# Kernel tuning notes

Hardware: AMD Instinct MI355X
Metric: run time of the kernel (lower is better)

Reference implementation:

```python
import jax, jax.numpy as jnp
import numpy as np


def setup_inputs() -> dict:
    key = jax.random.key(0)
    k1, k2, k3, k4 = jax.random.split(key, 4)
    B, T, N, D = 4, 8, 512, 256
    BT = B * T
    x = jax.random.normal(k1, (BT, N, D), dtype=jnp.float32)
    A_causal = jax.random.uniform(k2, (B, N, N), dtype=jnp.float32)
    W_qkv = jax.random.normal(k3, (3 * D, D), dtype=jnp.float32) * (D ** -0.5)
    W_proj = jax.random.normal(k4, (D, D), dtype=jnp.float32) * (D ** -0.5)
    b_proj = jnp.zeros((D,), dtype=jnp.float32)
    causal_lambda = jnp.ones((1,), dtype=jnp.float32) * 0.1
    return {
        "x": x,
        "A_causal": A_causal,
        "W_qkv": W_qkv,
        "W_proj": W_proj,
        "b_proj": b_proj,
        "causal_lambda": causal_lambda,
        "num_frames": 8,
    }


def reference(x, A_causal, W_qkv, W_proj, b_proj, causal_lambda, num_frames):
    BT, N, D = x.shape
    H = 8
    hd = D // H
    scale = hd ** -0.5
    # qkv projection (torch Linear: x @ W.T), split into q,k,v of shape [BT,H,N,hd]
    qkv = (x @ W_qkv.T).reshape(BT, N, 3, H, hd)
    qkv = jnp.transpose(qkv, (2, 0, 3, 1, 4))  # [3,BT,H,N,hd]
    q, k, v = qkv[0], qkv[1], qkv[2]
    attn = jnp.einsum("bhnd,bhmd->bhnm", q, k) * scale  # [BT,H,N,N]
    # expand A_causal [B,N,N] over frames (axis 0) and heads (broadcast axis 1)
    A_exp = jnp.repeat(A_causal, num_frames, axis=0)[:, None, :, :]  # [BT,1,N,N]
    attn = attn + causal_lambda[0] * A_exp
    attn = jax.nn.softmax(attn, axis=-1)
    out = jnp.einsum("bhnm,bhmd->bhnd", attn, v)  # [BT,H,N,hd]
    out = jnp.transpose(out, (0, 2, 1, 3)).reshape(BT, N, D)
    return out @ W_proj.T + b_proj
```

## Files before the change

kernel.cpp:

```cpp
#include <hip/hip_runtime.h>
#include <hip/hip_bf16.h>

typedef unsigned short u16;
typedef unsigned int   u32;
typedef __attribute__((ext_vector_type(8))) short short8;
typedef __attribute__((ext_vector_type(4))) float f32x4;

#define LOG2E 1.4426950408889634f
#define LDK 72

static __device__ __forceinline__ u16 f2b(float f) {
    u32 u = __float_as_uint(f);
    u += 0x7fffu + ((u >> 16) & 1u);
    return (u16)(u >> 16);
}
static __device__ __forceinline__ u32 pk2(float a, float b) {
    return (u32)f2b(a) | ((u32)f2b(b) << 16);
}
static __device__ __forceinline__ u32 cvtpk2(float a, float b) {
    u32 r;
    asm("v_cvt_pk_bf16_f32 %0, %1, %2" : "=v"(r) : "v"(b), "v"(a));
    return r;
}

__global__ __launch_bounds__(256) void prep(const float* __restrict__ X,
                                            const float* __restrict__ A,
                                            const float* __restrict__ LAM,
                                            const float* __restrict__ Wq,
                                            const float* __restrict__ Wp,
                                            u16* __restrict__ xb,
                                            u16* __restrict__ AB,
                                            u16* __restrict__ wqb,
                                            u16* __restrict__ wpb) {
    const int bid = blockIdx.x;
    const float* src;
    u16* dst;
    float scale;
    int base;
    if (bid < 2048)      { src = X;  dst = xb;  scale = 1.0f;            base = bid * 2048; }
    else if (bid < 2560) { src = A;  dst = AB;  scale = LAM[0] * LOG2E;  base = (bid - 2048) * 2048; }
    else if (bid < 2656) { src = Wq; dst = wqb; scale = 1.0f;            base = (bid - 2560) * 2048; }
    else                 { src = Wp; dst = wpb; scale = 1.0f;            base = (bid - 2656) * 2048; }
    const int i = base + threadIdx.x * 8;
    const float4 a = *(const float4*)(src + i);
    const float4 b = *(const float4*)(src + i + 4);
    uint4 o;
    o.x = pk2(scale * a.x, scale * a.y);
    o.y = pk2(scale * a.z, scale * a.w);
    o.z = pk2(scale * b.x, scale * b.y);
    o.w = pk2(scale * b.z, scale * b.w);
    *(uint4*)(dst + i) = o;
}

__global__ __launch_bounds__(256) void qkv_gemm(const u16* __restrict__ XB,
                                                const u16* __restrict__ WB,
                                                u16* __restrict__ qo,
                                                u16* __restrict__ ko,
                                                u16* __restrict__ vt) {
    __shared__ u16 SH[2 * 128 * LDK];
    u16* Xs = SH;
    u16* Ws = SH + 128 * LDK;
    const int t    = threadIdx.x;
    const int m0   = blockIdx.x << 7;
    const int o0   = blockIdx.y << 7;
    const int lane = t & 63;
    const int wid  = t >> 6;
    const int wr   = (wid >> 1) << 6;
    const int wc   = (wid & 1) << 6;
    const int ln   = lane & 15;
    const int quad = lane >> 4;

    const int r  = t >> 1;
    const int hf = (t & 1) << 5;
    const u16* xg = XB + (size_t)(m0 + r) * 256 + hf;
    const u16* wg = WB + (size_t)(o0 + r) * 256 + hf;
    uint4* xls = (uint4*)&Xs[r * LDK + hf];
    uint4* wls = (uint4*)&Ws[r * LDK + hf];

    f32x4 acc[4][4] = {};

    for (int kc = 0; kc < 256; kc += 64) {
        const uint4* xp = (const uint4*)(xg + kc);
        const uint4* wp = (const uint4*)(wg + kc);
        uint4 x0 = xp[0], x1 = xp[1], x2 = xp[2], x3 = xp[3];
        uint4 w0 = wp[0], w1 = wp[1], w2 = wp[2], w3 = wp[3];
        __syncthreads();
        xls[0] = x0; xls[1] = x1; xls[2] = x2; xls[3] = x3;
        wls[0] = w0; wls[1] = w1; wls[2] = w2; wls[3] = w3;
        __syncthreads();
#pragma unroll
        for (int kk = 0; kk < 64; kk += 32) {
            short8 a[4], b[4];
#pragma unroll
            for (int i = 0; i < 4; ++i)
                a[i] = *(const short8*)&Xs[(wr + i * 16 + ln) * LDK + kk + quad * 8];
#pragma unroll
            for (int j = 0; j < 4; ++j)
                b[j] = *(const short8*)&Ws[(wc + j * 16 + ln) * LDK + kk + quad * 8];
#pragma unroll
            for (int i = 0; i < 4; ++i)
#pragma unroll
                for (int j = 0; j < 4; ++j)
                    acc[i][j] = __builtin_amdgcn_mfma_f32_16x16x32_bf16(a[i], b[j], acc[i][j], 0, 0, 0);
        }
    }

    const int which = o0 >> 8;
    if (which < 2) {
        const float qscale = (which == 0) ? 0.17677669529663689f * LOG2E : 1.0f;
        u16* dst = (which == 0) ? qo : ko;
#pragma unroll
        for (int i = 0; i < 4; ++i) {
            const int mb = m0 + wr + i * 16 + quad * 4;
#pragma unroll
            for (int j = 0; j < 4; ++j) {
                const int o   = o0 + wc + j * 16 + ln;
                const int rem = o & 255;
                const int hh  = rem >> 5;
                const int dd  = rem & 31;
#pragma unroll
                for (int rr = 0; rr < 4; ++rr) {
                    const int m  = mb + rr;
                    const int bt = m >> 9;
                    const int n  = m & 511;
                    dst[(((size_t)bt * 8 + hh) * 512 + n) * 32 + dd] = f2b(acc[i][j][rr] * qscale);
                }
            }
        }
    } else {
        __syncthreads();
        u16* T = SH;
#pragma unroll
        for (int i = 0; i < 4; ++i) {
            const int ml = wr + i * 16 + quad * 4;
#pragma unroll
            for (int j = 0; j < 4; ++j) {
                const int ol = wc + j * 16 + ln;
                uint2 pv;
                pv.x = cvtpk2(acc[i][j][0], acc[i][j][1]);
                pv.y = cvtpk2(acc[i][j][2], acc[i][j][3]);
                *(uint2*)&T[ol * 136 + ml] = pv;
            }
        }
        __syncthreads();
        const int row = t >> 1;
        const int seg = (t & 1) << 6;
        const int o   = o0 + row;
        const int rem = o & 255;
        const int hh  = rem >> 5;
        const int dd  = rem & 31;
        const int bt  = m0 >> 9;
        u16* dstv = vt + (((size_t)bt * 8 + hh) * 32 + dd) * 512 + (m0 & 511) + seg;
#pragma unroll
        for (int kk2 = 0; kk2 < 8; ++kk2) {
            uint4 val = *(const uint4*)&T[row * 136 + seg + kk2 * 8];
            *(uint4*)(dstv + kk2 * 8) = val;
        }
    }
}

__global__ __launch_bounds__(256, 4) void attn_mfma(const u16* __restrict__ Q,
                                                    const u16* __restrict__ K,
                                                    const u16* __restrict__ VT,
                                                    const u16* __restrict__ AB,
                                                    const int* __restrict__ NF,
                                                    u16* __restrict__ AO) {
    __shared__ u16 Ks[2][64 * 40];
    __shared__ u16 Vs[2][32 * 72];
    __shared__ u16 Ps[4][32 * 40];
    const int t    = threadIdx.x;
    const int w    = t >> 6;
    const int lane = t & 63;
    const int ln   = lane & 15;
    const int quad = lane >> 4;
    const int L    = blockIdx.x;
    const int rr_  = L >> 3;
    const int qt   = rr_ & 3;
    const int h    = (rr_ >> 2) & 7;
    const int bt   = (L & 7) * 4 + (rr_ >> 5);
    const int bh   = bt * 8 + h;
    const int q0   = qt * 128 + w * 32;
    const size_t base = (size_t)bh * (512 * 32);
    const int b    = bt / NF[0];
    const u16* Ab  = AB + (size_t)b * 512 * 512;
    const u16* Ar0 = Ab + (size_t)(q0 + ln) * 512 + quad * 4;
    const u16* Ar1 = Ab + (size_t)(q0 + 16 + ln) * 512 + quad * 4;

    const int krow = t >> 2, kcol = (t & 3) * 8;
    const int vd   = t >> 3, vn   = (t & 7) * 8;
    const u16* Kg = K + base;
    const u16* Vg = VT + base;

    {
        uint4 s0 = *(const uint4*)(Kg + (size_t)krow * 32 + kcol);
        uint4 s2 = *(const uint4*)(Vg + (size_t)vd * 512 + vn);
        *(uint4*)&Ks[0][krow * 40 + kcol] = s0;
        *(uint4*)&Vs[0][vd * 72 + vn]     = s2;
    }
    uint2 ar[8];
#pragma unroll
    for (int mt = 0; mt < 4; ++mt) {
        ar[2*mt]     = *(const uint2*)(Ar0 + mt * 16);
        ar[2*mt + 1] = *(const uint2*)(Ar1 + mt * 16);
    }

    short8 qf[2];
#pragma unroll
    for (int nt = 0; nt < 2; ++nt)
        qf[nt] = *(const short8*)(Q + base + (size_t)(q0 + nt * 16 + ln) * 32 + quad * 8);

    f32x4 o[2][2] = {};
    float lsum0 = 0.f, lsum1 = 0.f;
    __syncthreads();

    int cur = 0;
    for (int jt = 0; jt < 512; jt += 64) {
        const int nxt = cur ^ 1;
        const int jn  = (jt + 64) & 511;
        uint4 t0 = *(const uint4*)(Kg + (size_t)(jn + krow) * 32 + kcol);
        uint4 t2 = *(const uint4*)(Vg + (size_t)vd * 512 + jn + vn);
        uint2 arn[8];
#pragma unroll
        for (int mt = 0; mt < 4; ++mt) {
            arn[2*mt]     = *(const uint2*)(Ar0 + jn + mt * 16);
            arn[2*mt + 1] = *(const uint2*)(Ar1 + jn + mt * 16);
        }

#pragma unroll
        for (int ks = 0; ks < 2; ++ks) {
#pragma unroll
            for (int mm = 0; mm < 2; ++mm) {
                const int mt = 2 * ks + mm;
                short8 ka = *(const short8*)&Ks[cur][(mt * 16 + ln) * 40 + quad * 8];
                f32x4 c0, c1;
                c0[0] = __uint_as_float(ar[2*mt].x << 16);   c0[1] = __uint_as_float(ar[2*mt].x & 0xffff0000u);
                c0[2] = __uint_as_float(ar[2*mt].y << 16);   c0[3] = __uint_as_float(ar[2*mt].y & 0xffff0000u);
                c1[0] = __uint_as_float(ar[2*mt+1].x << 16); c1[1] = __uint_as_float(ar[2*mt+1].x & 0xffff0000u);
                c1[2] = __uint_as_float(ar[2*mt+1].y << 16); c1[3] = __uint_as_float(ar[2*mt+1].y & 0xffff0000u);
                __builtin_amdgcn_s_setprio(1);
                const f32x4 s0 = __builtin_amdgcn_mfma_f32_16x16x32_bf16(ka, qf[0], c0, 0, 0, 0);
                const f32x4 s1 = __builtin_amdgcn_mfma_f32_16x16x32_bf16(ka, qf[1], c1, 0, 0, 0);
                __builtin_amdgcn_s_setprio(0);
                const float p00 = __builtin_amdgcn_exp2f(s0[0]), p01 = __builtin_amdgcn_exp2f(s0[1]);
                const float p02 = __builtin_amdgcn_exp2f(s0[2]), p03 = __builtin_amdgcn_exp2f(s0[3]);
                const float p10 = __builtin_amdgcn_exp2f(s1[0]), p11 = __builtin_amdgcn_exp2f(s1[1]);
                const float p12 = __builtin_amdgcn_exp2f(s1[2]), p13 = __builtin_amdgcn_exp2f(s1[3]);
                lsum0 += (p00 + p01) + (p02 + p03);
                lsum1 += (p10 + p11) + (p12 + p13);
                uint2 w0; w0.x = cvtpk2(p00, p01); w0.y = cvtpk2(p02, p03);
                uint2 w1; w1.x = cvtpk2(p10, p11); w1.y = cvtpk2(p12, p13);
                *(uint2*)&Ps[w][ln * 40 + mm * 16 + quad * 4]        = w0;
                *(uint2*)&Ps[w][(16 + ln) * 40 + mm * 16 + quad * 4] = w1;
            }
            short8 pa0 = *(const short8*)&Ps[w][ln * 40 + quad * 8];
            short8 pa1 = *(const short8*)&Ps[w][(16 + ln) * 40 + quad * 8];
            short8 vb0 = *(const short8*)&Vs[cur][ln * 72 + ks * 32 + quad * 8];
            short8 vb1 = *(const short8*)&Vs[cur][(16 + ln) * 72 + ks * 32 + quad * 8];
            __builtin_amdgcn_s_setprio(1);
            o[0][0] = __builtin_amdgcn_mfma_f32_16x16x32_bf16(pa0, vb0, o[0][0], 0, 0, 0);
            o[0][1] = __builtin_amdgcn_mfma_f32_16x16x32_bf16(pa0, vb1, o[0][1], 0, 0, 0);
            o[1][0] = __builtin_amdgcn_mfma_f32_16x16x32_bf16(pa1, vb0, o[1][0], 0, 0, 0);
            o[1][1] = __builtin_amdgcn_mfma_f32_16x16x32_bf16(pa1, vb1, o[1][1], 0, 0, 0);
            __builtin_amdgcn_s_setprio(0);
        }

        *(uint4*)&Ks[nxt][krow * 40 + kcol] = t0;
        *(uint4*)&Vs[nxt][vd * 72 + vn]     = t2;
        __syncthreads();
#pragma unroll
        for (int i = 0; i < 8; ++i) ar[i] = arn[i];
        cur = nxt;
    }

    lsum0 += __shfl_xor(lsum0, 16); lsum0 += __shfl_xor(lsum0, 32);
    lsum1 += __shfl_xor(lsum1, 16); lsum1 += __shfl_xor(lsum1, 32);
#pragma unroll
    for (int r = 0; r < 4; ++r) {
        const int src = quad * 4 + r;
        const float i0 = 1.f / __shfl(lsum0, src);
        const float i1 = 1.f / __shfl(lsum1, src);
        const int n0 = qt * 128 + w * 32 + quad * 4 + r;
#pragma unroll
        for (int ntd = 0; ntd < 2; ++ntd) {
            AO[((size_t)bt * 512 + n0) * 256 + h * 32 + ntd * 16 + ln]      = f2b(o[0][ntd][r] * i0);
            AO[((size_t)bt * 512 + n0 + 16) * 256 + h * 32 + ntd * 16 + ln] = f2b(o[1][ntd][r] * i1);
        }
    }
}

__global__ __launch_bounds__(256) void proj_gemm(const u16* __restrict__ X,
                                                 const u16* __restrict__ WB,
                                                 const float* __restrict__ BIAS,
                                                 float* __restrict__ OUT) {
    __shared__ u16 Xs[64 * LDK];
    __shared__ u16 Ws[128 * LDK];
    const int t    = threadIdx.x;
    const int m0   = blockIdx.x << 6;
    const int o0   = blockIdx.y << 7;
    const int lane = t & 63;
    const int wid  = t >> 6;
    const int wr   = (wid >> 1) << 5;
    const int wc   = (wid & 1) << 6;
    const int ln   = lane & 15;
    const int quad = lane >> 4;

    const int rx  = t >> 2;
    const int hx  = (t & 3) << 4;
    const int rw  = t >> 1;
    const int hw  = (t & 1) << 5;
    const u16* xg = X  + (size_t)(m0 + rx) * 256 + hx;
    const u16* wg = WB + (size_t)(o0 + rw) * 256 + hw;
    uint4* xls = (uint4*)&Xs[rx * LDK + hx];
    uint4* wls = (uint4*)&Ws[rw * LDK + hw];

    f32x4 acc[2][4] = {};

    for (int kc = 0; kc < 256; kc += 64) {
        const uint4* xp = (const uint4*)(xg + kc);
        const uint4* wp = (const uint4*)(wg + kc);
        uint4 x0 = xp[0], x1 = xp[1];
        uint4 w0 = wp[0], w1 = wp[1], w2 = wp[2], w3 = wp[3];
        __syncthreads();
        xls[0] = x0; xls[1] = x1;
        wls[0] = w0; wls[1] = w1; wls[2] = w2; wls[3] = w3;
        __syncthreads();
#pragma unroll
        for (int kk = 0; kk < 64; kk += 32) {
            short8 a[2], b[4];
#pragma unroll
            for (int i = 0; i < 2; ++i)
                a[i] = *(const short8*)&Xs[(wr + i * 16 + ln) * LDK + kk + quad * 8];
#pragma unroll
            for (int j = 0; j < 4; ++j)
                b[j] = *(const short8*)&Ws[(wc + j * 16 + ln) * LDK + kk + quad * 8];
#pragma unroll
            for (int i = 0; i < 2; ++i)
#pragma unroll
                for (int j = 0; j < 4; ++j)
                    acc[i][j] = __builtin_amdgcn_mfma_f32_16x16x32_bf16(a[i], b[j], acc[i][j], 0, 0, 0);
        }
    }

#pragma unroll
    for (int i = 0; i < 2; ++i) {
        const int mb = m0 + wr + i * 16 + quad * 4;
#pragma unroll
        for (int j = 0; j < 4; ++j) {
            const int o  = o0 + wc + j * 16 + ln;
            const float bo = BIAS[o];
#pragma unroll
            for (int rr = 0; rr < 4; ++rr) {
                const int m = mb + rr;
                OUT[(size_t)m * 256 + o] = acc[i][j][rr] + bo;
            }
        }
    }
}

extern "C" void kernel_launch(void* const* d_in, const int* in_sizes, int n_in,
                              void* d_out, int out_size, void* d_ws, size_t ws_size,
                              hipStream_t stream) {
    (void)in_sizes; (void)n_in; (void)out_size; (void)ws_size;
    const float* x     = (const float*)d_in[0];
    const float* A     = (const float*)d_in[1];
    const float* Wqkv  = (const float*)d_in[2];
    const float* Wproj = (const float*)d_in[3];
    const float* bproj = (const float*)d_in[4];
    const float* lam   = (const float*)d_in[5];
    const int*   nf    = (const int*)d_in[6];

    float* out = (float*)d_out;

    u16* q   = (u16*)d_ws;
    u16* k   = q + 4194304;
    u16* vt  = k + 4194304;
    u16* ao  = vt + 4194304;
    u16* xb  = ao + 4194304;
    u16* AB  = xb + 4194304;
    u16* wqb = AB + 1048576;
    u16* wpb = wqb + 196608;

    prep     <<<dim3(2688), 256, 0, stream>>>(x, A, lam, Wqkv, Wproj, xb, AB, wqb, wpb);
    qkv_gemm <<<dim3(128, 6), 256, 0, stream>>>(xb, wqb, q, k, vt);
    attn_mfma<<<dim3(1024), 256, 0, stream>>>(q, k, vt, AB, nf, ao);
    proj_gemm<<<dim3(256, 2), 256, 0, stream>>>(ao, wpb, bproj, out);
}
```

Measured before the change: 139.5 us.

## Fuse four kernels into one persistent kernel with software grid barriers

Merges the prep, QKV GEMM, attention and projection kernels into a single 1024-block kernel. The stages are separated by atomic-counter grid barriers, and a memset resets the barrier counter before launch. The goal is to remove per-launch overhead and the tail gaps between the four kernels. The cost is barrier spin time, some idle blocks in the GEMM stages, and a correctness risk: the barrier assumes all 1024 blocks are co-resident, and its timeout break could let a stage start early.

```diff
diff --git a/kernel.cpp b/kernel.cpp
--- a/kernel.cpp
+++ b/kernel.cpp
@@ -8,6 +8,7 @@
 
 #define LOG2E 1.4426950408889634f
 #define LDK 72
+#define GRIDN 1024u
 
 static __device__ __forceinline__ u16 f2b(float f) {
     u32 u = __float_as_uint(f);
@@ -23,335 +24,356 @@
     return r;
 }
 
-__global__ __launch_bounds__(256) void prep(const float* __restrict__ X,
-                                            const float* __restrict__ A,
-                                            const float* __restrict__ LAM,
-                                            const float* __restrict__ Wq,
-                                            const float* __restrict__ Wp,
-                                            u16* __restrict__ xb,
-                                            u16* __restrict__ AB,
-                                            u16* __restrict__ wqb,
-                                            u16* __restrict__ wpb) {
-    const int bid = blockIdx.x;
-    const float* src;
-    u16* dst;
-    float scale;
-    int base;
-    if (bid < 2048)      { src = X;  dst = xb;  scale = 1.0f;            base = bid * 2048; }
-    else if (bid < 2560) { src = A;  dst = AB;  scale = LAM[0] * LOG2E;  base = (bid - 2048) * 2048; }
-    else if (bid < 2656) { src = Wq; dst = wqb; scale = 1.0f;            base = (bid - 2560) * 2048; }
-    else                 { src = Wp; dst = wpb; scale = 1.0f;            base = (bid - 2656) * 2048; }
-    const int i = base + threadIdx.x * 8;
-    const float4 a = *(const float4*)(src + i);
-    const float4 b = *(const float4*)(src + i + 4);
-    uint4 o;
-    o.x = pk2(scale * a.x, scale * a.y);
-    o.y = pk2(scale * a.z, scale * a.w);
-    o.z = pk2(scale * b.x, scale * b.y);
-    o.w = pk2(scale * b.z, scale * b.w);
-    *(uint4*)(dst + i) = o;
-}
-
-__global__ __launch_bounds__(256) void qkv_gemm(const u16* __restrict__ XB,
-                                                const u16* __restrict__ WB,
-                                                u16* __restrict__ qo,
-                                                u16* __restrict__ ko,
-                                                u16* __restrict__ vt) {
+static __device__ __forceinline__ void gsync(u32* cnt, u32* flag, u32 phase) {
+    __syncthreads();
+    if (threadIdx.x == 0) {
+        __threadfence();
+        const u32 v = __hip_atomic_fetch_add(cnt, 1u, __ATOMIC_ACQ_REL, __HIP_MEMORY_SCOPE_AGENT);
+        if (v == phase * GRIDN - 1u) {
+            __hip_atomic_store(flag, phase, __ATOMIC_RELEASE, __HIP_MEMORY_SCOPE_AGENT);
+        } else {
+            int it = 0;
+            while (__hip_atomic_load(flag, __ATOMIC_ACQUIRE, __HIP_MEMORY_SCOPE_AGENT) < phase) {
+                __builtin_amdgcn_s_sleep(4);
+                if (++it > 300000) break;
+            }
+        }
+        __threadfence();
+    }
+    __syncthreads();
+}
+
+__global__ __launch_bounds__(256, 4) void mega(const float* __restrict__ X,
+                                               const float* __restrict__ A,
+                                               const float* __restrict__ LAM,
+                                               const float* __restrict__ Wq,
+                                               const float* __restrict__ Wp,
+                                               const float* __restrict__ BIAS,
+                                               const int*   __restrict__ NF,
+                                               u16* __restrict__ xb,
+                                               u16* __restrict__ AB,
+                                               u16* __restrict__ wqb,
+                                               u16* __restrict__ wpb,
+                                               u16* __restrict__ qo,
+                                               u16* __restrict__ ko,
+                                               u16* __restrict__ vt,
+                                               u16* __restrict__ ao,
+                                               float* __restrict__ OUT,
+                                               u32* __restrict__ BAR) {
     __shared__ u16 SH[2 * 128 * LDK];
-    u16* Xs = SH;
-    u16* Ws = SH + 128 * LDK;
-    const int t    = threadIdx.x;
-    const int m0   = blockIdx.x << 7;
-    const int o0   = blockIdx.y << 7;
-    const int lane = t & 63;
-    const int wid  = t >> 6;
-    const int wr   = (wid >> 1) << 6;
-    const int wc   = (wid & 1) << 6;
-    const int ln   = lane & 15;
-    const int quad = lane >> 4;
-
-    const int r  = t >> 1;
-    const int hf = (t & 1) << 5;
-    const u16* xg = XB + (size_t)(m0 + r) * 256 + hf;
-    const u16* wg = WB + (size_t)(o0 + r) * 256 + hf;
-    uint4* xls = (uint4*)&Xs[r * LDK + hf];
-    uint4* wls = (uint4*)&Ws[r * LDK + hf];
-
-    f32x4 acc[4][4] = {};
-
-    for (int kc = 0; kc < 256; kc += 64) {
-        const uint4* xp = (const uint4*)(xg + kc);
-        const uint4* wp = (const uint4*)(wg + kc);
-        uint4 x0 = xp[0], x1 = xp[1], x2 = xp[2], x3 = xp[3];
-        uint4 w0 = wp[0], w1 = wp[1], w2 = wp[2], w3 = wp[3];
+    u32* cnt  = BAR;
+    u32* flag = BAR + 32;
+    const int Bk = blockIdx.x;
+    const int t  = threadIdx.x;
+
+    {
+        const float s_ab = LAM[0] * LOG2E;
+        for (int u = Bk * 256 + t; u < 688128; u += 1024 * 256) {
+            const float* src; u16* dst; float sc; int off;
+            if (u < 524288)      { src = X;  dst = xb;  sc = 1.0f; off = u; }
+            else if (u < 655360) { src = A;  dst = AB;  sc = s_ab; off = u - 524288; }
+            else if (u < 679936) { src = Wq; dst = wqb; sc = 1.0f; off = u - 655360; }
+            else                 { src = Wp; dst = wpb; sc = 1.0f; off = u - 679936; }
+            const int i = off * 8;
+            const float4 a = *(const float4*)(src + i);
+            const float4 b = *(const float4*)(src + i + 4);
+            uint4 o;
+            o.x = pk2(sc * a.x, sc * a.y);
+            o.y = pk2(sc * a.z, sc * a.w);
+            o.z = pk2(sc * b.x, sc * b.y);
+            o.w = pk2(sc * b.z, sc * b.w);
+            *(uint4*)(dst + i) = o;
+        }
+    }
+    gsync(cnt, flag, 1);
+
+    if (Bk < 768) {
+        u16* Xs = SH;
+        u16* Ws = SH + 128 * LDK;
+        const int m0   = (Bk & 127) << 7;
+        const int o0   = (Bk >> 7) << 7;
+        const int lane = t & 63;
+        const int wid  = t >> 6;
+        const int wr   = (wid >> 1) << 6;
+        const int wc   = (wid & 1) << 6;
+        const int ln   = lane & 15;
+        const int quad = lane >> 4;
+
+        const int r  = t >> 1;
+        const int hf = (t & 1) << 5;
+        const u16* xg = xb  + (size_t)(m0 + r) * 256 + hf;
+        const u16* wg = wqb + (size_t)(o0 + r) * 256 + hf;
+        uint4* xls = (uint4*)&Xs[r * LDK + hf];
+        uint4* wls = (uint4*)&Ws[r * LDK + hf];
+
+        f32x4 acc[4][4] = {};
+
+        for (int kc = 0; kc < 256; kc += 64) {
+            const uint4* xp = (const uint4*)(xg + kc);
+            const uint4* wp = (const uint4*)(wg + kc);
+            uint4 x0 = xp[0], x1 = xp[1], x2 = xp[2], x3 = xp[3];
+            uint4 w0 = wp[0], w1 = wp[1], w2 = wp[2], w3 = wp[3];
+            __syncthreads();
+            xls[0] = x0; xls[1] = x1; xls[2] = x2; xls[3] = x3;
+            wls[0] = w0; wls[1] = w1; wls[2] = w2; wls[3] = w3;
+            __syncthreads();
+#pragma unroll
+            for (int kk = 0; kk < 64; kk += 32) {
+                short8 a[4], b[4];
+#pragma unroll
+                for (int i = 0; i < 4; ++i)
+                    a[i] = *(const short8*)&Xs[(wr + i * 16 + ln) * LDK + kk + quad * 8];
+#pragma unroll
+                for (int j = 0; j < 4; ++j)
+                    b[j] = *(const short8*)&Ws[(wc + j * 16 + ln) * LDK + kk + quad * 8];
+#pragma unroll
+                for (int i = 0; i < 4; ++i)
+#pragma unroll
+                    for (int j = 0; j < 4; ++j)
+                        acc[i][j] = __builtin_amdgcn_mfma_f32_16x16x32_bf16(a[i], b[j], acc[i][j], 0, 0, 0);
+            }
+        }
+
+        const int which = o0 >> 8;
+        if (which < 2) {
+            const float qscale = (which == 0) ? 0.17677669529663689f * LOG2E : 1.0f;
+            u16* dst = (which == 0) ? qo : ko;
+#pragma unroll
+            for (int i = 0; i < 4; ++i) {
+                const int mb = m0 + wr + i * 16 + quad * 4;
+#pragma unroll
+                for (int j = 0; j < 4; ++j) {
+                    const int o   = o0 + wc + j * 16 + ln;
+                    const int rem = o & 255;
+                    const int hh  = rem >> 5;
+                    const int dd  = rem & 31;
+#pragma unroll
+                    for (int rr = 0; rr < 4; ++rr) {
+                        const int m  = mb + rr;
+                        const int bt = m >> 9;
+                        const int n  = m & 511;
+                        dst[(((size_t)bt * 8 + hh) * 512 + n) * 32 + dd] = f2b(acc[i][j][rr] * qscale);
+                    }
+                }
+            }
+        } else {
+            __syncthreads();
+            u16* T = SH;
+#pragma unroll
+            for (int i = 0; i < 4; ++i) {
+                const int ml = wr + i * 16 + quad * 4;
+#pragma unroll
+                for (int j = 0; j < 4; ++j) {
+                    const int ol = wc + j * 16 + ln;
+                    uint2 pv;
+                    pv.x = cvtpk2(acc[i][j][0], acc[i][j][1]);
+                    pv.y = cvtpk2(acc[i][j][2], acc[i][j][3]);
+                    *(uint2*)&T[ol * 136 + ml] = pv;
+                }
+            }
+            __syncthreads();
+            const int row = t >> 1;
+            const int seg = (t & 1) << 6;
+            const int o   = o0 + row;
+            const int rem = o & 255;
+            const int hh  = rem >> 5;
+            const int dd  = rem & 31;
+            const int bt  = m0 >> 9;
+            u16* dstv = vt + (((size_t)bt * 8 + hh) * 32 + dd) * 512 + (m0 & 511) + seg;
+#pragma unroll
+            for (int kk2 = 0; kk2 < 8; ++kk2) {
+                uint4 val = *(const uint4*)&T[row * 136 + seg + kk2 * 8];
+                *(uint4*)(dstv + kk2 * 8) = val;
+            }
+        }
+    }
+    gsync(cnt, flag, 2);
+
+    {
+        u16 (*Ks)[64 * 40] = (u16 (*)[64 * 40])SH;
+        u16 (*Vs)[32 * 72] = (u16 (*)[32 * 72])(SH + 2 * 64 * 40);
+        u16 (*Ps)[32 * 40] = (u16 (*)[32 * 40])(SH + 2 * 64 * 40 + 2 * 32 * 72);
+        const int w    = t >> 6;
+        const int lane = t & 63;
+        const int ln   = lane & 15;
+        const int quad = lane >> 4;
+        const int L    = Bk;
+        const int rr_  = L >> 3;
+        const int qt   = rr_ & 3;
+        const int h    = (rr_ >> 2) & 7;
+        const int bt   = (L & 7) * 4 + (rr_ >> 5);
+        const int bh   = bt * 8 + h;
+        const int q0   = qt * 128 + w * 32;
+        const size_t base = (size_t)bh * (512 * 32);
+        const int b    = bt / NF[0];
+        const u16* Ab  = AB + (size_t)b * 512 * 512;
+        const u16* Ar0 = Ab + (size_t)(q0 + ln) * 512 + quad * 4;
+        const u16* Ar1 = Ab + (size_t)(q0 + 16 + ln) * 512 + quad * 4;
+
+        const int krow = t >> 2, kcol = (t & 3) * 8;
+        const int vd   = t >> 3, vn   = (t & 7) * 8;
+        const u16* Kg = ko + base;
+        const u16* Vg = vt + base;
+
+        {
+            uint4 s0 = *(const uint4*)(Kg + (size_t)krow * 32 + kcol);
+            uint4 s2 = *(const uint4*)(Vg + (size_t)vd * 512 + vn);
+            *(uint4*)&Ks[0][krow * 40 + kcol] = s0;
+            *(uint4*)&Vs[0][vd * 72 + vn]     = s2;
+        }
+        uint2 ar[8];
+#pragma unroll
+        for (int mt = 0; mt < 4; ++mt) {
+            ar[2*mt]     = *(const uint2*)(Ar0 + mt * 16);
+            ar[2*mt + 1] = *(const uint2*)(Ar1 + mt * 16);
+        }
+
+        short8 qf[2];
+#pragma unroll
+        for (int nt = 0; nt < 2; ++nt)
+            qf[nt] = *(const short8*)(qo + base + (size_t)(q0 + nt * 16 + ln) * 32 + quad * 8);
+
+        f32x4 o[2][2] = {};
+        float lsum0 = 0.f, lsum1 = 0.f;
         __syncthreads();
-        xls[0] = x0; xls[1] = x1; xls[2] = x2; xls[3] = x3;
-        wls[0] = w0; wls[1] = w1; wls[2] = w2; wls[3] = w3;
-        __syncthreads();
-#pragma unroll
-        for (int kk = 0; kk < 64; kk += 32) {
-            short8 a[4], b[4];
-#pragma unroll
-            for (int i = 0; i < 4; ++i)
-                a[i] = *(const short8*)&Xs[(wr + i * 16 + ln) * LDK + kk + quad * 8];
-#pragma unroll
-            for (int j = 0; j < 4; ++j)
-                b[j] = *(const short8*)&Ws[(wc + j * 16 + ln) * LDK + kk + quad * 8];
-#pragma unroll
-            for (int i = 0; i < 4; ++i)
+
+        int cur = 0;
+        for (int jt = 0; jt < 512; jt += 64) {
+            const int nxt = cur ^ 1;
+            const int jn  = (jt + 64) & 511;
+            uint4 t0 = *(const uint4*)(Kg + (size_t)(jn + krow) * 32 + kcol);
+            uint4 t2 = *(const uint4*)(Vg + (size_t)vd * 512 + jn + vn);
+            uint2 arn[8];
+#pragma unroll
+            for (int mt = 0; mt < 4; ++mt) {
+                arn[2*mt]     = *(const uint2*)(Ar0 + jn + mt * 16);
+                arn[2*mt + 1] = *(const uint2*)(Ar1 + jn + mt * 16);
+            }
+
+#pragma unroll
+            for (int ks = 0; ks < 2; ++ks) {
+#pragma unroll
+                for (int mm = 0; mm < 2; ++mm) {
+                    const int mt = 2 * ks + mm;
+                    short8 ka = *(const short8*)&Ks[cur][(mt * 16 + ln) * 40 + quad * 8];
+                    f32x4 c0, c1;
+                    c0[0] = __uint_as_float(ar[2*mt].x << 16);   c0[1] = __uint_as_float(ar[2*mt].x & 0xffff0000u);
+                    c0[2] = __uint_as_float(ar[2*mt].y << 16);   c0[3] = __uint_as_float(ar[2*mt].y & 0xffff0000u);
+                    c1[0] = __uint_as_float(ar[2*mt+1].x << 16); c1[1] = __uint_as_float(ar[2*mt+1].x & 0xffff0000u);
+                    c1[2] = __uint_as_float(ar[2*mt+1].y << 16); c1[3] = __uint_as_float(ar[2*mt+1].y & 0xffff0000u);
+                    __builtin_amdgcn_s_setprio(1);
+                    const f32x4 s0 = __builtin_amdgcn_mfma_f32_16x16x32_bf16(ka, qf[0], c0, 0, 0, 0);
+                    const f32x4 s1 = __builtin_amdgcn_mfma_f32_16x16x32_bf16(ka, qf[1], c1, 0, 0, 0);
+                    __builtin_amdgcn_s_setprio(0);
+                    const float p00 = __builtin_amdgcn_exp2f(s0[0]), p01 = __builtin_amdgcn_exp2f(s0[1]);
+                    const float p02 = __builtin_amdgcn_exp2f(s0[2]), p03 = __builtin_amdgcn_exp2f(s0[3]);
+                    const float p10 = __builtin_amdgcn_exp2f(s1[0]), p11 = __builtin_amdgcn_exp2f(s1[1]);
+                    const float p12 = __builtin_amdgcn_exp2f(s1[2]), p13 = __builtin_amdgcn_exp2f(s1[3]);
+                    lsum0 += (p00 + p01) + (p02 + p03);
+                    lsum1 += (p10 + p11) + (p12 + p13);
+                    uint2 w0; w0.x = cvtpk2(p00, p01); w0.y = cvtpk2(p02, p03);
+                    uint2 w1; w1.x = cvtpk2(p10, p11); w1.y = cvtpk2(p12, p13);
+                    *(uint2*)&Ps[w][ln * 40 + mm * 16 + quad * 4]        = w0;
+                    *(uint2*)&Ps[w][(16 + ln) * 40 + mm * 16 + quad * 4] = w1;
+                }
+                short8 pa0 = *(const short8*)&Ps[w][ln * 40 + quad * 8];
+                short8 pa1 = *(const short8*)&Ps[w][(16 + ln) * 40 + quad * 8];
+                short8 vb0 = *(const short8*)&Vs[cur][ln * 72 + ks * 32 + quad * 8];
+                short8 vb1 = *(const short8*)&Vs[cur][(16 + ln) * 72 + ks * 32 + quad * 8];
+                __builtin_amdgcn_s_setprio(1);
+                o[0][0] = __builtin_amdgcn_mfma_f32_16x16x32_bf16(pa0, vb0, o[0][0], 0, 0, 0);
+                o[0][1] = __builtin_amdgcn_mfma_f32_16x16x32_bf16(pa0, vb1, o[0][1], 0, 0, 0);
+                o[1][0] = __builtin_amdgcn_mfma_f32_16x16x32_bf16(pa1, vb0, o[1][0], 0, 0, 0);
+                o[1][1] = __builtin_amdgcn_mfma_f32_16x16x32_bf16(pa1, vb1, o[1][1], 0, 0, 0);
+                __builtin_amdgcn_s_setprio(0);
+            }
+
+            *(uint4*)&Ks[nxt][krow * 40 + kcol] = t0;
+            *(uint4*)&Vs[nxt][vd * 72 + vn]     = t2;
+            __syncthreads();
+#pragma unroll
+            for (int i = 0; i < 8; ++i) ar[i] = arn[i];
+            cur = nxt;
+        }
+
+        lsum0 += __shfl_xor(lsum0, 16); lsum0 += __shfl_xor(lsum0, 32);
+        lsum1 += __shfl_xor(lsum1, 16); lsum1 += __shfl_xor(lsum1, 32);
+#pragma unroll
+        for (int r = 0; r < 4; ++r) {
+            const int src = quad * 4 + r;
+            const float i0 = 1.f / __shfl(lsum0, src);
+            const float i1 = 1.f / __shfl(lsum1, src);
+            const int n0 = qt * 128 + w * 32 + quad * 4 + r;
+#pragma unroll
+            for (int ntd = 0; ntd < 2; ++ntd) {
+                ao[((size_t)bt * 512 + n0) * 256 + h * 32 + ntd * 16 + ln]      = f2b(o[0][ntd][r] * i0);
+                ao[((size_t)bt * 512 + n0 + 16) * 256 + h * 32 + ntd * 16 + ln] = f2b(o[1][ntd][r] * i1);
+            }
+        }
+    }
+    gsync(cnt, flag, 3);
+
+    if (Bk < 512) {
+        u16* Xs = SH;
+        u16* Ws = SH + 64 * LDK;
+        const int m0   = (Bk & 255) << 6;
+        const int o0   = (Bk >> 8) << 7;
+        const int lane = t & 63;
+        const int wid  = t >> 6;
+        const int wr   = (wid >> 1) << 5;
+        const int wc   = (wid & 1) << 6;
+        const int ln   = lane & 15;
+        const int quad = lane >> 4;
+
+        const int rx  = t >> 2;
+        const int hx  = (t & 3) << 4;
+        const int rw  = t >> 1;
+        const int hw  = (t & 1) << 5;
+        const u16* xg = ao  + (size_t)(m0 + rx) * 256 + hx;
+        const u16* wg = wpb + (size_t)(o0 + rw) * 256 + hw;
+        uint4* xls = (uint4*)&Xs[rx * LDK + hx];
+        uint4* wls = (uint4*)&Ws[rw * LDK + hw];
+
+        f32x4 acc[2][4] = {};
+
+        for (int kc = 0; kc < 256; kc += 64) {
+            const uint4* xp = (const uint4*)(xg + kc);
+            const uint4* wp = (const uint4*)(wg + kc);
+            uint4 x0 = xp[0], x1 = xp[1];
+            uint4 w0 = wp[0], w1 = wp[1], w2 = wp[2], w3 = wp[3];
+            __syncthreads();
+            xls[0] = x0; xls[1] = x1;
+            wls[0] = w0; wls[1] = w1; wls[2] = w2; wls[3] = w3;
+            __syncthreads();
+#pragma unroll
+            for (int kk = 0; kk < 64; kk += 32) {
+                short8 a[2], b[4];
+#pragma unroll
+                for (int i = 0; i < 2; ++i)
+                    a[i] = *(const short8*)&Xs[(wr + i * 16 + ln) * LDK + kk + quad * 8];
 #pragma unroll
                 for (int j = 0; j < 4; ++j)
-                    acc[i][j] = __builtin_amdgcn_mfma_f32_16x16x32_bf16(a[i], b[j], acc[i][j], 0, 0, 0);
-        }
-    }
-
-    const int which = o0 >> 8;
-    if (which < 2) {
-        const float qscale = (which == 0) ? 0.17677669529663689f * LOG2E : 1.0f;
-        u16* dst = (which == 0) ? qo : ko;
-#pragma unroll
-        for (int i = 0; i < 4; ++i) {
+                    b[j] = *(const short8*)&Ws[(wc + j * 16 + ln) * LDK + kk + quad * 8];
+#pragma unroll
+                for (int i = 0; i < 2; ++i)
+#pragma unroll
+                    for (int j = 0; j < 4; ++j)
+                        acc[i][j] = __builtin_amdgcn_mfma_f32_16x16x32_bf16(a[i], b[j], acc[i][j], 0, 0, 0);
+            }
+        }
+
+#pragma unroll
+        for (int i = 0; i < 2; ++i) {
             const int mb = m0 + wr + i * 16 + quad * 4;
 #pragma unroll
             for (int j = 0; j < 4; ++j) {
-                const int o   = o0 + wc + j * 16 + ln;
-                const int rem = o & 255;
-                const int hh  = rem >> 5;
-                const int dd  = rem & 31;
+                const int o  = o0 + wc + j * 16 + ln;
+                const float bo = BIAS[o];
 #pragma unroll
                 for (int rr = 0; rr < 4; ++rr) {
-                    const int m  = mb + rr;
-                    const int bt = m >> 9;
-                    const int n  = m & 511;
-                    dst[(((size_t)bt * 8 + hh) * 512 + n) * 32 + dd] = f2b(acc[i][j][rr] * qscale);
+                    const int m = mb + rr;
+                    OUT[(size_t)m * 256 + o] = acc[i][j][rr] + bo;
                 }
-            }
-        }
-    } else {
-        __syncthreads();
-        u16* T = SH;
-#pragma unroll
-        for (int i = 0; i < 4; ++i) {
-            const int ml = wr + i * 16 + quad * 4;
-#pragma unroll
-            for (int j = 0; j < 4; ++j) {
-                const int ol = wc + j * 16 + ln;
-                uint2 pv;
-                pv.x = cvtpk2(acc[i][j][0], acc[i][j][1]);
-                pv.y = cvtpk2(acc[i][j][2], acc[i][j][3]);
-                *(uint2*)&T[ol * 136 + ml] = pv;
-            }
-        }
-        __syncthreads();
-        const int row = t >> 1;
-        const int seg = (t & 1) << 6;
-        const int o   = o0 + row;
-        const int rem = o & 255;
-        const int hh  = rem >> 5;
-        const int dd  = rem & 31;
-        const int bt  = m0 >> 9;
-        u16* dstv = vt + (((size_t)bt * 8 + hh) * 32 + dd) * 512 + (m0 & 511) + seg;
-#pragma unroll
-        for (int kk2 = 0; kk2 < 8; ++kk2) {
-            uint4 val = *(const uint4*)&T[row * 136 + seg + kk2 * 8];
-            *(uint4*)(dstv + kk2 * 8) = val;
-        }
-    }
-}
-
-__global__ __launch_bounds__(256, 4) void attn_mfma(const u16* __restrict__ Q,
-                                                    const u16* __restrict__ K,
-                                                    const u16* __restrict__ VT,
-                                                    const u16* __restrict__ AB,
-                                                    const int* __restrict__ NF,
-                                                    u16* __restrict__ AO) {
-    __shared__ u16 Ks[2][64 * 40];
-    __shared__ u16 Vs[2][32 * 72];
-    __shared__ u16 Ps[4][32 * 40];
-    const int t    = threadIdx.x;
-    const int w    = t >> 6;
-    const int lane = t & 63;
-    const int ln   = lane & 15;
-    const int quad = lane >> 4;
-    const int L    = blockIdx.x;
-    const int rr_  = L >> 3;
-    const int qt   = rr_ & 3;
-    const int h    = (rr_ >> 2) & 7;
-    const int bt   = (L & 7) * 4 + (rr_ >> 5);
-    const int bh   = bt * 8 + h;
-    const int q0   = qt * 128 + w * 32;
-    const size_t base = (size_t)bh * (512 * 32);
-    const int b    = bt / NF[0];
-    const u16* Ab  = AB + (size_t)b * 512 * 512;
-    const u16* Ar0 = Ab + (size_t)(q0 + ln) * 512 + quad * 4;
-    const u16* Ar1 = Ab + (size_t)(q0 + 16 + ln) * 512 + quad * 4;
-
-    const int krow = t >> 2, kcol = (t & 3) * 8;
-    const int vd   = t >> 3, vn   = (t & 7) * 8;
-    const u16* Kg = K + base;
-    const u16* Vg = VT + base;
-
-    {
-        uint4 s0 = *(const uint4*)(Kg + (size_t)krow * 32 + kcol);
-        uint4 s2 = *(const uint4*)(Vg + (size_t)vd * 512 + vn);
-        *(uint4*)&Ks[0][krow * 40 + kcol] = s0;
-        *(uint4*)&Vs[0][vd * 72 + vn]     = s2;
-    }
-    uint2 ar[8];
-#pragma unroll
-    for (int mt = 0; mt < 4; ++mt) {
-        ar[2*mt]     = *(const uint2*)(Ar0 + mt * 16);
-        ar[2*mt + 1] = *(const uint2*)(Ar1 + mt * 16);
-    }
-
-    short8 qf[2];
-#pragma unroll
-    for (int nt = 0; nt < 2; ++nt)
-        qf[nt] = *(const short8*)(Q + base + (size_t)(q0 + nt * 16 + ln) * 32 + quad * 8);
-
-    f32x4 o[2][2] = {};
-    float lsum0 = 0.f, lsum1 = 0.f;
-    __syncthreads();
-
-    int cur = 0;
-    for (int jt = 0; jt < 512; jt += 64) {
-        const int nxt = cur ^ 1;
-        const int jn  = (jt + 64) & 511;
-        uint4 t0 = *(const uint4*)(Kg + (size_t)(jn + krow) * 32 + kcol);
-        uint4 t2 = *(const uint4*)(Vg + (size_t)vd * 512 + jn + vn);
-        uint2 arn[8];
-#pragma unroll
-        for (int mt = 0; mt < 4; ++mt) {
-            arn[2*mt]     = *(const uint2*)(Ar0 + jn + mt * 16);
-            arn[2*mt + 1] = *(const uint2*)(Ar1 + jn + mt * 16);
-        }
-
-#pragma unroll
-        for (int ks = 0; ks < 2; ++ks) {
-#pragma unroll
-            for (int mm = 0; mm < 2; ++mm) {
-                const int mt = 2 * ks + mm;
-                short8 ka = *(const short8*)&Ks[cur][(mt * 16 + ln) * 40 + quad * 8];
-                f32x4 c0, c1;
-                c0[0] = __uint_as_float(ar[2*mt].x << 16);   c0[1] = __uint_as_float(ar[2*mt].x & 0xffff0000u);
-                c0[2] = __uint_as_float(ar[2*mt].y << 16);   c0[3] = __uint_as_float(ar[2*mt].y & 0xffff0000u);
-                c1[0] = __uint_as_float(ar[2*mt+1].x << 16); c1[1] = __uint_as_float(ar[2*mt+1].x & 0xffff0000u);
-                c1[2] = __uint_as_float(ar[2*mt+1].y << 16); c1[3] = __uint_as_float(ar[2*mt+1].y & 0xffff0000u);
-                __builtin_amdgcn_s_setprio(1);
-                const f32x4 s0 = __builtin_amdgcn_mfma_f32_16x16x32_bf16(ka, qf[0], c0, 0, 0, 0);
-                const f32x4 s1 = __builtin_amdgcn_mfma_f32_16x16x32_bf16(ka, qf[1], c1, 0, 0, 0);
-                __builtin_amdgcn_s_setprio(0);
-                const float p00 = __builtin_amdgcn_exp2f(s0[0]), p01 = __builtin_amdgcn_exp2f(s0[1]);
-                const float p02 = __builtin_amdgcn_exp2f(s0[2]), p03 = __builtin_amdgcn_exp2f(s0[3]);
-                const float p10 = __builtin_amdgcn_exp2f(s1[0]), p11 = __builtin_amdgcn_exp2f(s1[1]);
-                const float p12 = __builtin_amdgcn_exp2f(s1[2]), p13 = __builtin_amdgcn_exp2f(s1[3]);
-                lsum0 += (p00 + p01) + (p02 + p03);
-                lsum1 += (p10 + p11) + (p12 + p13);
-                uint2 w0; w0.x = cvtpk2(p00, p01); w0.y = cvtpk2(p02, p03);
-                uint2 w1; w1.x = cvtpk2(p10, p11); w1.y = cvtpk2(p12, p13);
-                *(uint2*)&Ps[w][ln * 40 + mm * 16 + quad * 4]        = w0;
-                *(uint2*)&Ps[w][(16 + ln) * 40 + mm * 16 + quad * 4] = w1;
-            }
-            short8 pa0 = *(const short8*)&Ps[w][ln * 40 + quad * 8];
-            short8 pa1 = *(const short8*)&Ps[w][(16 + ln) * 40 + quad * 8];
-            short8 vb0 = *(const short8*)&Vs[cur][ln * 72 + ks * 32 + quad * 8];
-            short8 vb1 = *(const short8*)&Vs[cur][(16 + ln) * 72 + ks * 32 + quad * 8];
-            __builtin_amdgcn_s_setprio(1);
-            o[0][0] = __builtin_amdgcn_mfma_f32_16x16x32_bf16(pa0, vb0, o[0][0], 0, 0, 0);
-            o[0][1] = __builtin_amdgcn_mfma_f32_16x16x32_bf16(pa0, vb1, o[0][1], 0, 0, 0);
-            o[1][0] = __builtin_amdgcn_mfma_f32_16x16x32_bf16(pa1, vb0, o[1][0], 0, 0, 0);
-            o[1][1] = __builtin_amdgcn_mfma_f32_16x16x32_bf16(pa1, vb1, o[1][1], 0, 0, 0);
-            __builtin_amdgcn_s_setprio(0);
-        }
-
-        *(uint4*)&Ks[nxt][krow * 40 + kcol] = t0;
-        *(uint4*)&Vs[nxt][vd * 72 + vn]     = t2;
-        __syncthreads();
-#pragma unroll
-        for (int i = 0; i < 8; ++i) ar[i] = arn[i];
-        cur = nxt;
-    }
-
-    lsum0 += __shfl_xor(lsum0, 16); lsum0 += __shfl_xor(lsum0, 32);
-    lsum1 += __shfl_xor(lsum1, 16); lsum1 += __shfl_xor(lsum1, 32);
-#pragma unroll
-    for (int r = 0; r < 4; ++r) {
-        const int src = quad * 4 + r;
-        const float i0 = 1.f / __shfl(lsum0, src);
-        const float i1 = 1.f / __shfl(lsum1, src);
-        const int n0 = qt * 128 + w * 32 + quad * 4 + r;
-#pragma unroll
-        for (int ntd = 0; ntd < 2; ++ntd) {
-            AO[((size_t)bt * 512 + n0) * 256 + h * 32 + ntd * 16 + ln]      = f2b(o[0][ntd][r] * i0);
-            AO[((size_t)bt * 512 + n0 + 16) * 256 + h * 32 + ntd * 16 + ln] = f2b(o[1][ntd][r] * i1);
-        }
-    }
-}
-
-__global__ __launch_bounds__(256) void proj_gemm(const u16* __restrict__ X,
-                                                 const u16* __restrict__ WB,
-                                                 const float* __restrict__ BIAS,
-                                                 float* __restrict__ OUT) {
-    __shared__ u16 Xs[64 * LDK];
-    __shared__ u16 Ws[128 * LDK];
-    const int t    = threadIdx.x;
-    const int m0   = blockIdx.x << 6;
-    const int o0   = blockIdx.y << 7;
-    const int lane = t & 63;
-    const int wid  = t >> 6;
-    const int wr   = (wid >> 1) << 5;
-    const int wc   = (wid & 1) << 6;
-    const int ln   = lane & 15;
-    const int quad = lane >> 4;
-
-    const int rx  = t >> 2;
-    const int hx  = (t & 3) << 4;
-    const int rw  = t >> 1;
-    const int hw  = (t & 1) << 5;
-    const u16* xg = X  + (size_t)(m0 + rx) * 256 + hx;
-    const u16* wg = WB + (size_t)(o0 + rw) * 256 + hw;
-    uint4* xls = (uint4*)&Xs[rx * LDK + hx];
-    uint4* wls = (uint4*)&Ws[rw * LDK + hw];
-
-    f32x4 acc[2][4] = {};
-
-    for (int kc = 0; kc < 256; kc += 64) {
-        const uint4* xp = (const uint4*)(xg + kc);
-        const uint4* wp = (const uint4*)(wg + kc);
-        uint4 x0 = xp[0], x1 = xp[1];
-        uint4 w0 = wp[0], w1 = wp[1], w2 = wp[2], w3 = wp[3];
-        __syncthreads();
-        xls[0] = x0; xls[1] = x1;
-        wls[0] = w0; wls[1] = w1; wls[2] = w2; wls[3] = w3;
-        __syncthreads();
-#pragma unroll
-        for (int kk = 0; kk < 64; kk += 32) {
-            short8 a[2], b[4];
-#pragma unroll
-            for (int i = 0; i < 2; ++i)
-                a[i] = *(const short8*)&Xs[(wr + i * 16 + ln) * LDK + kk + quad * 8];
-#pragma unroll
-            for (int j = 0; j < 4; ++j)
-                b[j] = *(const short8*)&Ws[(wc + j * 16 + ln) * LDK + kk + quad * 8];
-#pragma unroll
-            for (int i = 0; i < 2; ++i)
-#pragma unroll
-                for (int j = 0; j < 4; ++j)
-                    acc[i][j] = __builtin_amdgcn_mfma_f32_16x16x32_bf16(a[i], b[j], acc[i][j], 0, 0, 0);
-        }
-    }
-
-#pragma unroll
-    for (int i = 0; i < 2; ++i) {
-        const int mb = m0 + wr + i * 16 + quad * 4;
-#pragma unroll
-        for (int j = 0; j < 4; ++j) {
-            const int o  = o0 + wc + j * 16 + ln;
-            const float bo = BIAS[o];
-#pragma unroll
-            for (int rr = 0; rr < 4; ++rr) {
-                const int m = mb + rr;
-                OUT[(size_t)m * 256 + o] = acc[i][j][rr] + bo;
             }
         }
     }
@@ -379,9 +401,9 @@
     u16* AB  = xb + 4194304;
     u16* wqb = AB + 1048576;
     u16* wpb = wqb + 196608;
-
-    prep     <<<dim3(2688), 256, 0, stream>>>(x, A, lam, Wqkv, Wproj, xb, AB, wqb, wpb);
-    qkv_gemm <<<dim3(128, 6), 256, 0, stream>>>(xb, wqb, q, k, vt);
-    attn_mfma<<<dim3(1024), 256, 0, stream>>>(q, k, vt, AB, nf, ao);
-    proj_gemm<<<dim3(256, 2), 256, 0, stream>>>(ao, wpb, bproj, out);
-}
+    u32* bar = (u32*)(wpb + 65536);
+
+    hipMemsetAsync(bar, 0, 256, stream);
+    mega<<<dim3(GRIDN), 256, 0, stream>>>(x, A, lam, Wqkv, Wproj, bproj, nf,
+                                          xb, AB, wqb, wpb, q, k, vt, ao, out, bar);
+}
```

New measurement: 527.9 us. +278.5%, slower.
